# Kernel tuning notes

Hardware: AMD Instinct MI355X
Metric: run time of the kernel (lower is better)

Reference implementation:

```python
import jax, jax.numpy as jnp
import numpy as np

PRECISION = 2.0 ** 24  # ctx._precision stand-in; factor = sqrt(precision)
SF_CONST = 48.0


def setup_inputs() -> dict:
    key = jax.random.key(0)
    k1, k2, k3 = jax.random.split(key, 3)
    x = jax.random.normal(k1, (16, 128, 128, 128), dtype=jnp.float32)  # NCHW
    W = jax.random.normal(k2, (256, 128, 3, 3), dtype=jnp.float32) * 0.05  # OIHW
    b = jax.random.normal(k3, (256,), dtype=jnp.float32) * 0.1
    return {"x": x, "W": W, "b": b}


def reference(x, W, b):
    # --- quantize() (standard, non-mixture path) ---
    N = float(np.prod(W.shape[1:]))           # in_ch * kh * kw = 1152
    factor = np.sqrt(PRECISION)               # sqrt(ctx._precision)
    sf = np.sqrt(SF_CONST / N)
    w_sum = jnp.sum(jnp.abs(W), axis=(1, 2, 3))          # [O]
    w_sum = jnp.where(w_sum == 0, 1.0, w_sum)
    fw = (factor / sf - np.sqrt(N / 12.0) * 5.0) / w_sum  # [O]
    Wq = jnp.round(W * fw[:, None, None, None])

    # --- forward int-quantized conv ---
    x_max = jnp.max(jnp.abs(x))
    fx = jnp.where(x_max > 0, (factor * sf - 0.5) / x_max, 1.0)
    xq = jnp.round(fx * x)
    y = jax.lax.conv_general_dilated(
        xq, Wq,
        window_strides=(1, 1),
        padding=((1, 1), (1, 1)),
        dimension_numbers=("NCHW", "OIHW", "NCHW"),
    )
    # dequantize per output channel, then fused float bias add
    y = y / (fx * fw[:, None, None]) + b[:, None, None]
    # Activation (ReLU); BN disabled, dropout disabled in this config
    return jax.nn.relu(y)
```

## Files before the change

### kernel.cpp

```cpp
#include <hip/hip_runtime.h>
#include <math.h>


#define FW_NUM 20017.23017802413f
#define FX_NUM 835.5924988699913f
#define WQA_OFF 2048
#define WQB_OFF (640 * 1024)
#define XQ_OFF  (2 * 1024 * 1024)
#define XQ_BYTES 67108864ull

#define CK  16
#define CKP 24
#define JW  130

typedef _Float16 half8 __attribute__((ext_vector_type(8)));
typedef _Float16 half4 __attribute__((ext_vector_type(4)));
typedef float floatx16 __attribute__((ext_vector_type(16)));

__device__ __forceinline__ void gl_lds16(const void* g, void* s) {
    __builtin_amdgcn_global_load_lds((const __attribute__((address_space(1))) void*)g,
                                     (__attribute__((address_space(3))) void*)s, 16, 0, 0);
}

__global__ void xmax_kernel(const float* __restrict__ x, unsigned int* wsu, int n4) {
    int tid = blockIdx.x * blockDim.x + threadIdx.x;
    int stride = gridDim.x * blockDim.x;
    const float4* x4 = (const float4*)x;
    float m = 0.f;
    for (int i = tid; i < n4; i += stride) {
        float4 v = x4[i];
        m = fmaxf(m, fmaxf(fmaxf(fabsf(v.x), fabsf(v.y)), fmaxf(fabsf(v.z), fabsf(v.w))));
    }
    #pragma unroll
    for (int off = 32; off >= 1; off >>= 1)
        m = fmaxf(m, __shfl_down(m, off, 64));
    __shared__ float sm[4];
    if ((threadIdx.x & 63) == 0) sm[threadIdx.x >> 6] = m;
    __syncthreads();
    if (threadIdx.x == 0) {
        m = fmaxf(fmaxf(sm[0], sm[1]), fmaxf(sm[2], sm[3]));
        atomicMax(wsu, __float_as_uint(m));
    }
}

__global__ void wq_kernel(const float* __restrict__ W, float* wsf, int big) {
    int o = blockIdx.x;
    int t = threadIdx.x;
    const float* wrow = W + o * 1152;
    float wv[9];
    float s = 0.f;
    #pragma unroll
    for (int k = 0; k < 9; k++) { wv[k] = wrow[t * 9 + k]; s += fabsf(wv[k]); }
    #pragma unroll
    for (int off = 32; off >= 1; off >>= 1) s += __shfl_down(s, off, 64);
    __shared__ float sred[2];
    __shared__ float sfw;
    if ((t & 63) == 0) sred[t >> 6] = s;
    __syncthreads();
    if (t == 0) {
        float wsum = sred[0] + sred[1];
        if (wsum == 0.f) wsum = 1.f;
        float fw = FW_NUM / wsum;
        wsf[64 + o] = fw;
        sfw = fw;
    }
    __syncthreads();
    float fw = sfw;
    _Float16* wqa = (_Float16*)((char*)wsf + WQA_OFF);
    _Float16* wqb = (_Float16*)((char*)wsf + WQB_OFF);
    #pragma unroll
    for (int k = 0; k < 9; k++) {
        _Float16 hv = (_Float16)rintf(wv[k] * fw);
        wqa[(o * 9 + k) * 128 + t] = hv;
        if (big)
            wqb[(((t >> 4) * 9 + k) * 256 + o) * 16 + (t & 15)] = hv;
    }
}

__global__ void quantx_kernel(const float* __restrict__ x, const float* __restrict__ wsf,
                              _Float16* __restrict__ xq) {
    int bid = blockIdx.x;
    int h  = bid & 127;
    int cc = (bid >> 7) & 7;
    int n  = bid >> 10;
    float xmax = __uint_as_float(((const unsigned int*)wsf)[0]);
    float fx = xmax > 0.f ? FX_NUM / xmax : 1.0f;
    int w = threadIdx.x;
    const float* xp = x + ((size_t)(n * 128 + cc * 16) * 128 + h) * 128 + w;
    half8 v0, v1;
    #pragma unroll
    for (int ci = 0; ci < 8; ci++)  v0[ci] = (_Float16)rintf(fx * xp[(size_t)ci * 16384]);
    #pragma unroll
    for (int ci = 8; ci < 16; ci++) v1[ci - 8] = (_Float16)rintf(fx * xp[(size_t)ci * 16384]);
    _Float16* op = xq + ((size_t)bid * 128 + w) * 16;
    *(half8*)op = v0;
    *(half8*)(op + 8) = v1;
}

__global__ __launch_bounds__(256, 2) void conv_main(const _Float16* __restrict__ xq,
                                                    const float* __restrict__ bias,
                                                    const float* __restrict__ wsf,
                                                    float* __restrict__ out) {
    __shared__ __align__(16) _Float16 xs[2][10 * 66 * 16];
    __shared__ __align__(16) _Float16 wl[2][9 * 64 * 16];
    __shared__ float sc[64], bz[64];

    float xmax = __uint_as_float(((const unsigned int*)wsf)[0]);
    float fx = xmax > 0.f ? FX_NUM / xmax : 1.0f;

    int bx = blockIdx.x;
    int o0 = (bx & 3) << 6;
    int w0 = ((bx >> 2) & 1) << 6;
    int h0 = ((bx >> 3) & 15) << 3;
    int n  = bx >> 7;

    int tid = threadIdx.x;
    int lane = tid & 63;
    int wv = tid >> 6;
    int m32 = lane & 31;
    int q2 = lane >> 5;

    const char* wqb = (const char*)wsf + WQB_OFF;

    {
        uint4 z = {0u, 0u, 0u, 0u};
        uint4* p = (uint4*)xs;
        for (int i = tid; i < (int)(sizeof(xs) / 16); i += 256) p[i] = z;
        if (tid < 64) {
            float fwv = wsf[64 + o0 + tid];
            sc[tid] = 1.0f / (fx * fwv);
            bz[tid] = bias[o0 + tid];
        }
    }
    __syncthreads();

    floatx16 acc[2][4];
    #pragma unroll
    for (int a1 = 0; a1 < 2; a1++)
        #pragma unroll
        for (int a2 = 0; a2 < 4; a2++)
            #pragma unroll
            for (int e = 0; e < 16; e++) acc[a1][a2][e] = 0.f;

    auto stage_async = [&](int ccs, int tb) {
        for (int s = wv; s < 38; s += 4) {
            if (s < 20) {
                int r = s >> 1, hseg = s & 1;
                int h = h0 + r - 1;
                if (h >= 0 && h < 128) {
                    size_t pix = ((size_t)((n * 8 + ccs) * 128 + h)) * 128 + w0;
                    const char* src = (const char*)xq + pix * 32 + hseg * 1024 + (size_t)lane * 16;
                    char* dst = (char*)&xs[tb][(r * 66 + 1) * 16] + hseg * 1024;
                    gl_lds16(src, dst);
                }
            } else {
                int t2 = s - 20, tap = t2 >> 1, g = t2 & 1;
                const char* src = wqb + ((size_t)(ccs * 9 + tap) * 256 + o0) * 32 + g * 1024 + (size_t)lane * 16;
                char* dst = (char*)&wl[tb][tap * 64 * 16] + g * 1024;
                gl_lds16(src, dst);
            }
        }
    };
    auto halo_load = [&](int ccs) -> half8 {
        half8 v = {};
        if (tid < 40) {
            int r = tid >> 2, sd = (tid >> 1) & 1, g = tid & 1;
            int h = h0 + r - 1;
            int wh = sd ? (w0 + 64) : (w0 - 1);
            if (h >= 0 && h < 128 && wh >= 0 && wh < 128)
                v = *(const half8*)(xq + (((size_t)((n * 8 + ccs) * 128 + h)) * 128 + wh) * 16 + g * 8);
        }
        return v;
    };
    auto halo_store = [&](int tb, half8 v) {
        if (tid < 40) {
            int r = tid >> 2, sd = (tid >> 1) & 1, g = tid & 1;
            int h = h0 + r - 1;
            int wh = sd ? (w0 + 64) : (w0 - 1);
            if (h >= 0 && h < 128 && wh >= 0 && wh < 128)
                *(half8*)&xs[tb][(r * 66 + (sd ? 65 : 0)) * 16 + g * 8] = v;
        }
    };

    {
        half8 hv = halo_load(0);
        stage_async(0, 0);
        halo_store(0, hv);
    }
    __syncthreads();

    for (int cc = 0; cc < 8; ++cc) {
        int cb = cc & 1;
        half8 hn = {};
        if (cc < 7) {
            hn = halo_load(cc + 1);
            stage_async(cc + 1, cb ^ 1);
        }

        #pragma unroll
        for (int kh = 0; kh < 3; ++kh) {
            #pragma unroll
            for (int kw = 0; kw < 3; ++kw) {
                int tap = kh * 3 + kw;
                const _Float16* wp = &wl[cb][(tap * 64 + m32) * 16 + q2 * 8];
                half8 wf0 = *(const half8*)wp;
                half8 wf1 = *(const half8*)(wp + 32 * 16);
                #pragma unroll
                for (int pt = 0; pt < 4; ++pt) {
                    const _Float16* xp =
                        &xs[cb][(((wv * 2 + (pt >> 1) + kh) * 66) + (pt & 1) * 32 + m32 + kw) * 16 + q2 * 8];
                    half8 xf = *(const half8*)xp;
                    acc[0][pt] = __builtin_amdgcn_mfma_f32_32x32x16_f16(wf0, xf, acc[0][pt], 0, 0, 0);
                    acc[1][pt] = __builtin_amdgcn_mfma_f32_32x32x16_f16(wf1, xf, acc[1][pt], 0, 0, 0);
                }
            }
        }

        if (cc < 7) halo_store(cb ^ 1, hn);
        __syncthreads();
    }

    #pragma unroll
    for (int ot = 0; ot < 2; ++ot) {
        #pragma unroll
        for (int e = 0; e < 16; ++e) {
            int o_loc = ot * 32 + (e & 3) + 8 * (e >> 2) + 4 * q2;
            float scale = sc[o_loc];
            float bv = bz[o_loc];
            #pragma unroll
            for (int pt = 0; pt < 4; ++pt) {
                int h = h0 + wv * 2 + (pt >> 1);
                int w = w0 + (pt & 1) * 32 + m32;
                float v = fmaxf(fmaf(acc[ot][pt][e], scale, bv), 0.f);
                out[(((size_t)(n * 256 + o0 + o_loc)) * 128 + h) * 128 + w] = v;
            }
        }
    }
}

__global__ __launch_bounds__(256, 2) void conv_fallback(const float* __restrict__ x,
                                                        const float* __restrict__ bias,
                                                        const float* __restrict__ wsf,
                                                        float* __restrict__ out) {
    __shared__ __align__(16) _Float16 xs[6 * JW * CKP];
    __shared__ __align__(16) _Float16 wlds[9 * 64 * CKP];

    const unsigned int* wsu = (const unsigned int*)wsf;
    float xmax = __uint_as_float(wsu[0]);
    float fx = xmax > 0.f ? FX_NUM / xmax : 1.0f;

    int bx = blockIdx.x;
    int n  = bx >> 5;
    int h0 = (bx & 31) << 2;
    int o0 = blockIdx.y << 6;

    int tid  = threadIdx.x;
    int lane = tid & 63;
    int wave = tid >> 6;
    int m32  = lane & 31;
    int q2   = lane >> 5;

    const _Float16* wq16 = (const _Float16*)((const char*)wsf + WQA_OFF);
    const float* xn = x + (size_t)n * (128 * 128 * 128);

    floatx16 acc[4][2];
    #pragma unroll
    for (int mt = 0; mt < 4; mt++)
        #pragma unroll
        for (int nt = 0; nt < 2; nt++)
            #pragma unroll
            for (int e = 0; e < 16; e++) acc[mt][nt][e] = 0.f;

    if (tid < 192) {
        int r = tid >> 5;
        int s = tid & 31;
        int c = s & 15;
        int j = (s >> 4) ? (JW - 1) : 0;
        xs[(r * JW + j) * CKP + c] = (_Float16)0.f;
    }

    for (int c0 = 0; c0 < 128; c0 += CK) {
        __syncthreads();
        #pragma unroll
        for (int it = 0; it < 12; ++it) {
            int idx = tid + it * 256;
            int j  = (idx & 127) + 1;
            int c4 = (idx >> 7) & 3;
            int r  = idx >> 9;
            int h  = h0 + r - 1;
            float v0 = 0.f, v1 = 0.f, v2 = 0.f, v3 = 0.f;
            if (h >= 0 && h < 128) {
                const float* xp = xn + (size_t)(c0 + c4 * 4) * 16384 + h * 128 + (j - 1);
                v0 = xp[0]; v1 = xp[16384]; v2 = xp[32768]; v3 = xp[49152];
            }
            half4 hv;
            hv[0] = (_Float16)rintf(fx * v0);
            hv[1] = (_Float16)rintf(fx * v1);
            hv[2] = (_Float16)rintf(fx * v2);
            hv[3] = (_Float16)rintf(fx * v3);
            *(half4*)&xs[(r * JW + j) * CKP + c4 * 4] = hv;
        }
        #pragma unroll
        for (int it = 0; it < 5; ++it) {
            int idx = tid + it * 256;
            if (idx < 1152) {
                int o   = idx / 18;
                int rem = idx - o * 18;
                int tap = rem >> 1;
                int g   = rem & 1;
                half8 v = *(const half8*)(wq16 + ((size_t)(o0 + o) * 9 + tap) * 128 + c0 + g * 8);
                *(half8*)&wlds[(tap * 64 + o) * CKP + g * 8] = v;
            }
        }
        __syncthreads();

        const _Float16* xbase = &xs[(wave * JW + m32) * CKP + q2 * 8];
        const _Float16* wbase = &wlds[m32 * CKP + q2 * 8];
        #pragma unroll
        for (int kh = 0; kh < 3; ++kh) {
            #pragma unroll
            for (int kw = 0; kw < 3; ++kw) {
                int tap = kh * 3 + kw;
                half8 b0 = *(const half8*)(wbase + (tap * 64 +  0) * CKP);
                half8 b1 = *(const half8*)(wbase + (tap * 64 + 32) * CKP);
                #pragma unroll
                for (int mt = 0; mt < 4; ++mt) {
                    half8 a = *(const half8*)(xbase + (kh * JW + kw + mt * 32) * CKP);
                    acc[mt][0] = __builtin_amdgcn_mfma_f32_32x32x16_f16(a, b0, acc[mt][0], 0, 0, 0);
                    acc[mt][1] = __builtin_amdgcn_mfma_f32_32x32x16_f16(a, b1, acc[mt][1], 0, 0, 0);
                }
            }
        }
    }

    int h = h0 + wave;
    #pragma unroll
    for (int nt = 0; nt < 2; ++nt) {
        int o = o0 + nt * 32 + m32;
        float fwv = wsf[64 + o];
        float scale = 1.0f / (fx * fwv);
        float bv = bias[o];
        float* op = out + (((size_t)n * 256 + o) * 128 + h) * 128;
        #pragma unroll
        for (int mt = 0; mt < 4; ++mt) {
            #pragma unroll
            for (int g = 0; g < 4; ++g) {
                int w = mt * 32 + 8 * g + 4 * q2;
                float4 r;
                r.x = fmaxf(fmaf(acc[mt][nt][4 * g + 0], scale, bv), 0.f);
                r.y = fmaxf(fmaf(acc[mt][nt][4 * g + 1], scale, bv), 0.f);
                r.z = fmaxf(fmaf(acc[mt][nt][4 * g + 2], scale, bv), 0.f);
                r.w = fmaxf(fmaf(acc[mt][nt][4 * g + 3], scale, bv), 0.f);
                *(float4*)(op + w) = r;
            }
        }
    }
}

extern "C" void kernel_launch(void* const* d_in, const int* in_sizes, int n_in,
                              void* d_out, int out_size, void* d_ws, size_t ws_size,
                              hipStream_t stream) {
    const float* x = (const float*)d_in[0];
    const float* W = (const float*)d_in[1];
    const float* b = (const float*)d_in[2];
    float* out = (float*)d_out;
    float* wsf = (float*)d_ws;

    int big = (ws_size >= (size_t)XQ_OFF + XQ_BYTES) ? 1 : 0;

    hipMemsetAsync(d_ws, 0, 256, stream);

    xmax_kernel<<<1024, 256, 0, stream>>>(x, (unsigned int*)d_ws, (16 * 128 * 128 * 128) / 4);
    wq_kernel<<<256, 128, 0, stream>>>(W, wsf, big);

    if (big) {
        _Float16* xq = (_Float16*)((char*)d_ws + XQ_OFF);
        quantx_kernel<<<16 * 8 * 128, 128, 0, stream>>>(x, wsf, xq);
        conv_main<<<2048, 256, 0, stream>>>(xq, b, wsf, out);
    } else {
        dim3 grid(512, 4);
        conv_fallback<<<grid, 256, 0, stream>>>(x, b, wsf, out);
    }
}
```

Baseline: 495.3 us.

## Retile conv to 16x32 spatial tiles with swizzled LDS and row reuse

Changes the conv_main output tile from 8x64 to 16x32 pixels so each wave covers four rows. Six input rows are loaded per kw and reused across the three kh taps instead of reloading per tap. An XOR swizzle is applied to the weight and activation LDS layouts to reduce bank conflicts, and blocks are remapped across the grid. The costs are a larger halo (more halo threads, taller tile) and more complex index arithmetic.

```diff
diff --git a/kernel.cpp b/kernel.cpp
--- a/kernel.cpp
+++ b/kernel.cpp
@@ -68,12 +68,17 @@
     float fw = sfw;
     _Float16* wqa = (_Float16*)((char*)wsf + WQA_OFF);
     _Float16* wqb = (_Float16*)((char*)wsf + WQB_OFF);
+    int oswz = (o & ~3) | ((o & 3) ^ ((o >> 3) & 3));
+    int qflip = (o >> 2) & 1;
     #pragma unroll
     for (int k = 0; k < 9; k++) {
         _Float16 hv = (_Float16)rintf(wv[k] * fw);
         wqa[(o * 9 + k) * 128 + t] = hv;
-        if (big)
-            wqb[(((t >> 4) * 9 + k) * 256 + o) * 16 + (t & 15)] = hv;
+        if (big) {
+            int q = (t >> 3) & 1;
+            int qswz = q ^ qflip;
+            wqb[(((t >> 4) * 9 + k) * 256 + oswz) * 16 + qswz * 8 + (t & 7)] = hv;
+        }
     }
 }
 
@@ -101,17 +106,18 @@
                                                     const float* __restrict__ bias,
                                                     const float* __restrict__ wsf,
                                                     float* __restrict__ out) {
-    __shared__ __align__(16) _Float16 xs[2][10 * 66 * 16];
+    __shared__ __align__(16) _Float16 xs[2][18 * 34 * 16];
     __shared__ __align__(16) _Float16 wl[2][9 * 64 * 16];
     __shared__ float sc[64], bz[64];
 
     float xmax = __uint_as_float(((const unsigned int*)wsf)[0]);
     float fx = xmax > 0.f ? FX_NUM / xmax : 1.0f;
 
-    int bx = blockIdx.x;
+    int bx0 = blockIdx.x;
+    int bx = (bx0 & 7) * 256 + (bx0 >> 3);
     int o0 = (bx & 3) << 6;
-    int w0 = ((bx >> 2) & 1) << 6;
-    int h0 = ((bx >> 3) & 15) << 3;
+    int w0 = ((bx >> 2) & 3) << 5;
+    int h0 = ((bx >> 4) & 7) << 4;
     int n  = bx >> 7;
 
     int tid = threadIdx.x;
@@ -121,6 +127,23 @@
     int q2 = lane >> 5;
 
     const char* wqb = (const char*)wsf + WQB_OFF;
+
+    int xcol[3];
+    #pragma unroll
+    for (int kw = 0; kw < 3; ++kw) {
+        int j = m32 + kw;
+        xcol[kw] = (j * 32 + q2 * 16) ^ ((((j) >> 2) & 7) << 4);
+    }
+    int wcol = (m32 * 32 + q2 * 16) ^ (((m32 >> 2) & 7) << 4);
+
+    int xsrcoff;
+    {
+        int jp = 1 + (lane >> 1), qp = lane & 1;
+        int t = (jp >> 3) & 3;
+        int j = (jp & ~3) | ((jp & 3) ^ t);
+        int q = qp ^ ((jp >> 2) & 1);
+        xsrcoff = (j - 1) * 32 + q * 16;
+    }
 
     {
         uint4 z = {0u, 0u, 0u, 0u};
@@ -143,18 +166,18 @@
             for (int e = 0; e < 16; e++) acc[a1][a2][e] = 0.f;
 
     auto stage_async = [&](int ccs, int tb) {
-        for (int s = wv; s < 38; s += 4) {
-            if (s < 20) {
-                int r = s >> 1, hseg = s & 1;
+        for (int s = wv; s < 36; s += 4) {
+            if (s < 18) {
+                int r = s;
                 int h = h0 + r - 1;
                 if (h >= 0 && h < 128) {
                     size_t pix = ((size_t)((n * 8 + ccs) * 128 + h)) * 128 + w0;
-                    const char* src = (const char*)xq + pix * 32 + hseg * 1024 + (size_t)lane * 16;
-                    char* dst = (char*)&xs[tb][(r * 66 + 1) * 16] + hseg * 1024;
+                    const char* src = (const char*)xq + pix * 32 + xsrcoff;
+                    char* dst = (char*)&xs[tb][(r * 34 + 1) * 16];
                     gl_lds16(src, dst);
                 }
             } else {
-                int t2 = s - 20, tap = t2 >> 1, g = t2 & 1;
+                int t2 = s - 18, tap = t2 >> 1, g = t2 & 1;
                 const char* src = wqb + ((size_t)(ccs * 9 + tap) * 256 + o0) * 32 + g * 1024 + (size_t)lane * 16;
                 char* dst = (char*)&wl[tb][tap * 64 * 16] + g * 1024;
                 gl_lds16(src, dst);
@@ -163,22 +186,22 @@
     };
     auto halo_load = [&](int ccs) -> half8 {
         half8 v = {};
-        if (tid < 40) {
+        if (tid < 72) {
             int r = tid >> 2, sd = (tid >> 1) & 1, g = tid & 1;
             int h = h0 + r - 1;
-            int wh = sd ? (w0 + 64) : (w0 - 1);
+            int wh = sd ? (w0 + 32) : (w0 - 1);
             if (h >= 0 && h < 128 && wh >= 0 && wh < 128)
                 v = *(const half8*)(xq + (((size_t)((n * 8 + ccs) * 128 + h)) * 128 + wh) * 16 + g * 8);
         }
         return v;
     };
     auto halo_store = [&](int tb, half8 v) {
-        if (tid < 40) {
+        if (tid < 72) {
             int r = tid >> 2, sd = (tid >> 1) & 1, g = tid & 1;
             int h = h0 + r - 1;
-            int wh = sd ? (w0 + 64) : (w0 - 1);
+            int wh = sd ? (w0 + 32) : (w0 - 1);
             if (h >= 0 && h < 128 && wh >= 0 && wh < 128)
-                *(half8*)&xs[tb][(r * 66 + (sd ? 65 : 0)) * 16 + g * 8] = v;
+                *(half8*)((char*)&xs[tb][0] + r * 1088 + (sd ? 33 * 32 : 0) + g * 16) = v;
         }
     };
 
@@ -197,21 +220,23 @@
             stage_async(cc + 1, cb ^ 1);
         }
 
-        #pragma unroll
-        for (int kh = 0; kh < 3; ++kh) {
-            #pragma unroll
-            for (int kw = 0; kw < 3; ++kw) {
-                int tap = kh * 3 + kw;
-                const _Float16* wp = &wl[cb][(tap * 64 + m32) * 16 + q2 * 8];
+        const char* xb = (const char*)&xs[cb][0] + wv * (4 * 1088);
+        const char* wb = (const char*)&wl[cb][0];
+        #pragma unroll
+        for (int kw = 0; kw < 3; ++kw) {
+            half8 xf[6];
+            #pragma unroll
+            for (int srow = 0; srow < 6; ++srow)
+                xf[srow] = *(const half8*)(xb + srow * 1088 + xcol[kw]);
+            #pragma unroll
+            for (int kh = 0; kh < 3; ++kh) {
+                const char* wp = wb + (kh * 3 + kw) * 2048 + wcol;
                 half8 wf0 = *(const half8*)wp;
-                half8 wf1 = *(const half8*)(wp + 32 * 16);
+                half8 wf1 = *(const half8*)(wp + 1024);
                 #pragma unroll
-                for (int pt = 0; pt < 4; ++pt) {
-                    const _Float16* xp =
-                        &xs[cb][(((wv * 2 + (pt >> 1) + kh) * 66) + (pt & 1) * 32 + m32 + kw) * 16 + q2 * 8];
-                    half8 xf = *(const half8*)xp;
-                    acc[0][pt] = __builtin_amdgcn_mfma_f32_32x32x16_f16(wf0, xf, acc[0][pt], 0, 0, 0);
-                    acc[1][pt] = __builtin_amdgcn_mfma_f32_32x32x16_f16(wf1, xf, acc[1][pt], 0, 0, 0);
+                for (int p = 0; p < 4; ++p) {
+                    acc[0][p] = __builtin_amdgcn_mfma_f32_32x32x16_f16(wf0, xf[p + kh], acc[0][p], 0, 0, 0);
+                    acc[1][p] = __builtin_amdgcn_mfma_f32_32x32x16_f16(wf1, xf[p + kh], acc[1][p], 0, 0, 0);
                 }
             }
         }
@@ -228,11 +253,10 @@
             float scale = sc[o_loc];
             float bv = bz[o_loc];
             #pragma unroll
-            for (int pt = 0; pt < 4; ++pt) {
-                int h = h0 + wv * 2 + (pt >> 1);
-                int w = w0 + (pt & 1) * 32 + m32;
-                float v = fmaxf(fmaf(acc[ot][pt][e], scale, bv), 0.f);
-                out[(((size_t)(n * 256 + o0 + o_loc)) * 128 + h) * 128 + w] = v;
+            for (int p = 0; p < 4; ++p) {
+                int h = h0 + wv * 4 + p;
+                float v = fmaxf(fmaf(acc[ot][p][e], scale, bv), 0.f);
+                out[(((size_t)(n * 256 + o0 + o_loc)) * 128 + h) * 128 + w0 + m32] = v;
             }
         }
     }
```

Result: no change. 501.0 us (+1.1%).
